# Kernel tuning notes

Measured on AMD Instinct MI355X. Metric: run time of the kernel, lower is better.

The kernel has to match this reference:

```python
import jax, jax.numpy as jnp
import numpy as np

B, N, M = 8, 2048, 2048
DQ = DK = DV = H = O = 1024

def setup_inputs() -> dict:
    key = jax.random.key(0)
    ks = jax.random.split(key, 10)
    input_query = jax.random.normal(ks[0], (B, N, DQ), dtype=jnp.float32)
    input_key = jax.random.normal(ks[1], (B, M, DK), dtype=jnp.float32)
    input_value = jax.random.normal(ks[2], (B, M, DV), dtype=jnp.float32)
    seq_lens = jax.random.randint(ks[3], (B,), 1, M + 1)
    seq_lens = seq_lens.at[0].set(M)  # original asserts max(seq_lens) == M
    s = 1.0 / np.sqrt(DQ)
    Wq = jax.random.normal(ks[4], (DQ, H), dtype=jnp.float32) * s
    bq = jnp.zeros((H,), dtype=jnp.float32)
    Wk = jax.random.normal(ks[5], (DK, H), dtype=jnp.float32) * s
    bk = jnp.zeros((H,), dtype=jnp.float32)
    Wv = jax.random.normal(ks[6], (DV, O), dtype=jnp.float32) * s
    bv = jnp.zeros((O,), dtype=jnp.float32)
    return {"input_query": input_query, "input_key": input_key, "input_value": input_value,
            "seq_lens": seq_lens, "Wq": Wq, "bq": bq, "Wk": Wk, "bk": bk, "Wv": Wv, "bv": bv}


def reference(input_query, input_key, input_value, seq_lens, Wq, bq, Wk, bk, Wv, bv):
    hidden_dim = Wq.shape[1]
    lq = input_query @ Wq + bq          # (B, N, H)
    lk = input_key @ Wk + bk            # (B, M, H)
    lv = input_value @ Wv + bv          # (B, M, O)
    scores = jnp.einsum('bnh,bmh->bnm', lq, lk) / jnp.sqrt(jnp.float32(hidden_dim))
    # additive mask: 0 for valid positions, finfo.min for padded (as in original)
    valid = (jnp.arange(scores.shape[-1]) < seq_lens[:, None])[:, None, :]  # (B,1,M)
    add_mask = jnp.where(valid, 0.0, jnp.finfo(scores.dtype).min)
    scores = scores + add_mask
    probs = jax.nn.softmax(scores, axis=-1)
    out = jnp.einsum('bnm,bmo->bno', probs, lv)  # dropout is identity in eval
    return out
```

## Files before the change

### kernel.cpp

```cpp
#include <hip/hip_runtime.h>
#include <hip/hip_bf16.h>

typedef unsigned short u16;
typedef __attribute__((ext_vector_type(8))) short bfrag;
typedef __attribute__((ext_vector_type(4))) float f32x4;
typedef __attribute__((ext_vector_type(8))) unsigned short us8;
typedef __attribute__((ext_vector_type(4))) unsigned short us4;

__device__ __forceinline__ u16 f2bf(float f) {
  union { float f; unsigned int u; } x; x.f = f;
  unsigned int r = x.u + 0x7fffu + ((x.u >> 16) & 1u);
  return (u16)(r >> 16);
}
__device__ __forceinline__ float bf2f(u16 u) {
  union { unsigned int u; float f; } x; x.u = ((unsigned int)u) << 16;
  return x.f;
}

__device__ __forceinline__ void gld16(const void* g, void* l) {
  __builtin_amdgcn_global_load_lds((const __attribute__((address_space(1))) void*)g,
                                   (__attribute__((address_space(3))) void*)l, 16, 0, 0);
}

__global__ __launch_bounds__(256) void transpose_w(const float* __restrict__ W0,
                                                   const float* __restrict__ W1,
                                                   const float* __restrict__ W2,
                                                   u16* __restrict__ T0,
                                                   u16* __restrict__ T1,
                                                   u16* __restrict__ T2) {
  const float* W = (blockIdx.z == 0) ? W0 : ((blockIdx.z == 1) ? W1 : W2);
  u16* T = (blockIdx.z == 0) ? T0 : ((blockIdx.z == 1) ? T1 : T2);
  __shared__ u16 tile[64][72];
  const int t = threadIdx.x;
  const int rr = t >> 4;
  const int cc = (t & 15) * 4;
  const int kbase = blockIdx.y * 64, nbase = blockIdx.x * 64;
#pragma unroll
  for (int j = 0; j < 4; ++j) {
    int kl = rr + j * 16;
    float4 v = *(const float4*)(W + (size_t)(kbase + kl) * 1024 + nbase + cc);
    tile[kl][cc + 0] = f2bf(v.x);
    tile[kl][cc + 1] = f2bf(v.y);
    tile[kl][cc + 2] = f2bf(v.z);
    tile[kl][cc + 3] = f2bf(v.w);
  }
  __syncthreads();
#pragma unroll
  for (int j = 0; j < 4; ++j) {
    int nl = rr + j * 16;
    us4 o;
    o[0] = tile[cc + 0][nl];
    o[1] = tile[cc + 1][nl];
    o[2] = tile[cc + 2][nl];
    o[3] = tile[cc + 3][nl];
    *(us4*)(T + (size_t)(nbase + nl) * 1024 + kbase + cc) = o;
  }
}

__global__ __launch_bounds__(256) void cvt_bf16(const float* __restrict__ src,
                                                u16* __restrict__ dst, int n8) {
  int i = blockIdx.x * blockDim.x + threadIdx.x;
  const int stride = gridDim.x * blockDim.x;
  for (; i < n8; i += stride) {
    const float4* p = (const float4*)(src + (size_t)i * 8);
    float4 v0 = p[0], v1 = p[1];
    us8 o;
    o[0] = f2bf(v0.x); o[1] = f2bf(v0.y); o[2] = f2bf(v0.z); o[3] = f2bf(v0.w);
    o[4] = f2bf(v1.x); o[5] = f2bf(v1.y); o[6] = f2bf(v1.z); o[7] = f2bf(v1.w);
    *(us8*)(dst + (size_t)i * 8) = o;
  }
}

template <int OUT>
__global__ __launch_bounds__(512, 2) void gemm256(const u16* __restrict__ gA,
                                                  const u16* __restrict__ gB,
                                                  const float* __restrict__ bias,
                                                  void* __restrict__ outp,
                                                  int K, int ldc,
                                                  size_t aStride, size_t bStride,
                                                  size_t cStride) {
  __shared__ u16 lds[65536];
  const int tid = threadIdx.x;
  const int z = blockIdx.z;
  const u16* A = gA + (size_t)z * aStride;
  const u16* B = gB + (size_t)z * bStride;
  const int brow = blockIdx.y * 256, bcol = blockIdx.x * 256;

  const int wv = tid >> 6, l = tid & 63;
  const int wm = wv >> 2, wn = wv & 3;
  const int fr = l & 15, fq = l >> 4;
  const int g0 = (fq ^ (fr & 7)) * 8;
  const int g1 = ((4 + fq) ^ (fr & 7)) * 8;

  const int srow = tid >> 3;
  const int sg = (tid & 7) ^ (srow & 7);
  const u16* aS = A + (size_t)(brow + srow) * K + sg * 8;
  const u16* bS = B + (size_t)(bcol + srow) * K + sg * 8;
  u16* const dA = lds + (tid >> 6) * 512;
  u16* const dB = lds + 32768 + (tid >> 6) * 512;

  f32x4 acc[8][4] = {};
  const int NT = K >> 6;

#pragma unroll
  for (int c = 0; c < 4; ++c) gld16(aS + (size_t)c * 64 * K, dA + c * 4096);
#pragma unroll
  for (int c = 0; c < 4; ++c) gld16(bS + (size_t)c * 64 * K, dB + c * 4096);
  asm volatile("s_waitcnt vmcnt(0)" ::: "memory");
  __builtin_amdgcn_s_barrier();

  for (int s = 0; s < NT; ++s) {
    const int cur = s & 1;
    const u16* At = lds + cur * 16384;
    const u16* Bt = lds + 32768 + cur * 16384;

    if (s + 1 < NT) {
      const int nb = cur ^ 1;
      const size_t ko = (size_t)(s + 1) * 64;
#pragma unroll
      for (int c = 0; c < 4; ++c)
        gld16(aS + ko + (size_t)c * 64 * K, dA + nb * 16384 + c * 4096);
#pragma unroll
      for (int c = 0; c < 4; ++c)
        gld16(bS + ko + (size_t)c * 64 * K, dB + nb * 16384 + c * 4096);
    }

    bfrag a[4][2], b[2][2][2];
#pragma unroll
    for (int m = 0; m < 4; ++m) {
      const u16* p = At + (wm * 128 + m * 16 + fr) * 64;
      a[m][0] = *(const bfrag*)(p + g0);
      a[m][1] = *(const bfrag*)(p + g1);
    }
#pragma unroll
    for (int n = 0; n < 2; ++n) {
      const u16* p = Bt + (wn * 64 + n * 16 + fr) * 64;
      b[0][n][0] = *(const bfrag*)(p + g0);
      b[0][n][1] = *(const bfrag*)(p + g1);
    }
    __builtin_amdgcn_s_barrier();
    __builtin_amdgcn_s_setprio(1);
#pragma unroll
    for (int n = 0; n < 2; ++n)
#pragma unroll
      for (int m = 0; m < 4; ++m) {
        acc[m][n] = __builtin_amdgcn_mfma_f32_16x16x32_bf16(a[m][0], b[0][n][0], acc[m][n], 0, 0, 0);
        acc[m][n] = __builtin_amdgcn_mfma_f32_16x16x32_bf16(a[m][1], b[0][n][1], acc[m][n], 0, 0, 0);
      }
    __builtin_amdgcn_s_setprio(0);
    __builtin_amdgcn_s_barrier();

#pragma unroll
    for (int n = 0; n < 2; ++n) {
      const u16* p = Bt + (wn * 64 + 32 + n * 16 + fr) * 64;
      b[1][n][0] = *(const bfrag*)(p + g0);
      b[1][n][1] = *(const bfrag*)(p + g1);
    }
    __builtin_amdgcn_s_barrier();
    __builtin_amdgcn_s_setprio(1);
#pragma unroll
    for (int n = 0; n < 2; ++n)
#pragma unroll
      for (int m = 0; m < 4; ++m) {
        acc[m][2 + n] = __builtin_amdgcn_mfma_f32_16x16x32_bf16(a[m][0], b[1][n][0], acc[m][2 + n], 0, 0, 0);
        acc[m][2 + n] = __builtin_amdgcn_mfma_f32_16x16x32_bf16(a[m][1], b[1][n][1], acc[m][2 + n], 0, 0, 0);
      }
    __builtin_amdgcn_s_setprio(0);
    __builtin_amdgcn_s_barrier();

#pragma unroll
    for (int m = 0; m < 4; ++m) {
      const u16* p = At + (wm * 128 + 64 + m * 16 + fr) * 64;
      a[m][0] = *(const bfrag*)(p + g0);
      a[m][1] = *(const bfrag*)(p + g1);
    }
    __builtin_amdgcn_s_barrier();
    __builtin_amdgcn_s_setprio(1);
#pragma unroll
    for (int n = 0; n < 2; ++n)
#pragma unroll
      for (int m = 0; m < 4; ++m) {
        acc[4 + m][n] = __builtin_amdgcn_mfma_f32_16x16x32_bf16(a[m][0], b[0][n][0], acc[4 + m][n], 0, 0, 0);
        acc[4 + m][n] = __builtin_amdgcn_mfma_f32_16x16x32_bf16(a[m][1], b[0][n][1], acc[4 + m][n], 0, 0, 0);
      }
    __builtin_amdgcn_s_setprio(0);
    __builtin_amdgcn_s_barrier();

    __builtin_amdgcn_s_setprio(1);
#pragma unroll
    for (int n = 0; n < 2; ++n)
#pragma unroll
      for (int m = 0; m < 4; ++m) {
        acc[4 + m][2 + n] = __builtin_amdgcn_mfma_f32_16x16x32_bf16(a[m][0], b[1][n][0], acc[4 + m][2 + n], 0, 0, 0);
        acc[4 + m][2 + n] = __builtin_amdgcn_mfma_f32_16x16x32_bf16(a[m][1], b[1][n][1], acc[4 + m][2 + n], 0, 0, 0);
      }
    __builtin_amdgcn_s_setprio(0);

    asm volatile("s_waitcnt vmcnt(0)" ::: "memory");
    __builtin_amdgcn_s_barrier();
  }

#pragma unroll
  for (int mg = 0; mg < 8; ++mg) {
    const int r0 = brow + wm * 128 + mg * 16 + fq * 4;
#pragma unroll
    for (int n = 0; n < 4; ++n) {
      const int c = bcol + wn * 64 + n * 16 + fr;
      f32x4 vv = acc[mg][n];
      if constexpr (OUT == 0) {
        float bb = bias[c];
        u16* C = (u16*)outp;
#pragma unroll
        for (int j = 0; j < 4; ++j) C[(size_t)(r0 + j) * ldc + c] = f2bf(vv[j] + bb);
      } else if constexpr (OUT == 1) {
        u16* C = (u16*)outp + (size_t)z * cStride;
#pragma unroll
        for (int j = 0; j < 4; ++j) C[(size_t)(r0 + j) * ldc + c] = f2bf(vv[j] * 0.03125f);
      } else if constexpr (OUT == 2) {
        float bb = bias[c];
        const int bz = r0 >> 11, mm = r0 & 2047;
        us4 o;
#pragma unroll
        for (int j = 0; j < 4; ++j) o[j] = f2bf(vv[j] + bb);
        *(us4*)((u16*)outp + ((size_t)bz * 1024 + c) * 2048 + mm) = o;
      } else {
        float* C = (float*)outp + (size_t)z * cStride;
#pragma unroll
        for (int j = 0; j < 4; ++j) C[(size_t)(r0 + j) * ldc + c] = vv[j];
      }
    }
  }
}

__global__ __launch_bounds__(256) void softmax_mask(u16* __restrict__ probs,
                                                    const int* __restrict__ seq) {
  const int bid = blockIdx.x;
  const int b = bid >> 11, n = bid & 2047;
  const int len = seq[b];
  u16* row = probs + ((size_t)b * 2048 + n) * 2048;
  const int t = threadIdx.x;
  const int w = t >> 6, l = t & 63;

  us8 sv = *(const us8*)(row + t * 8);
  float vals[8];
  float vmax = -1e30f;
#pragma unroll
  for (int e = 0; e < 8; ++e) {
    int m = t * 8 + e;
    float x = bf2f(sv[e]);
    vals[e] = (m < len) ? x : -1e30f;
    vmax = fmaxf(vmax, vals[e]);
  }
#pragma unroll
  for (int o = 32; o > 0; o >>= 1) vmax = fmaxf(vmax, __shfl_xor(vmax, o, 64));
  __shared__ float sm[4], ss[4];
  if (l == 0) sm[w] = vmax;
  __syncthreads();
  vmax = fmaxf(fmaxf(sm[0], sm[1]), fmaxf(sm[2], sm[3]));

  float ev[8];
  float sum = 0.f;
#pragma unroll
  for (int e = 0; e < 8; ++e) {
    int m = t * 8 + e;
    float p = (m < len) ? __expf(vals[e] - vmax) : 0.f;
    ev[e] = p;
    sum += p;
  }
#pragma unroll
  for (int o = 32; o > 0; o >>= 1) sum += __shfl_xor(sum, o, 64);
  if (l == 0) ss[w] = sum;
  __syncthreads();
  sum = ss[0] + ss[1] + ss[2] + ss[3];
  float inv = 1.f / sum;
  us8 ov;
#pragma unroll
  for (int e = 0; e < 8; ++e) ov[e] = f2bf(ev[e] * inv);
  *(us8*)(row + t * 8) = ov;
}

extern "C" void kernel_launch(void* const* d_in, const int* in_sizes, int n_in,
                              void* d_out, int out_size, void* d_ws, size_t ws_size,
                              hipStream_t stream) {
  const float* q   = (const float*)d_in[0];
  const float* k   = (const float*)d_in[1];
  const float* v   = (const float*)d_in[2];
  const int*   seq = (const int*)d_in[3];
  const float* Wq  = (const float*)d_in[4];
  const float* bq  = (const float*)d_in[5];
  const float* Wk  = (const float*)d_in[6];
  const float* bk  = (const float*)d_in[7];
  const float* Wv  = (const float*)d_in[8];
  const float* bv  = (const float*)d_in[9];
  float* out = (float*)d_out;

  u16* ws = (u16*)d_ws;
  u16* wtq = ws;
  u16* wtk = wtq + (size_t)1024 * 1024;
  u16* wtv = wtk + (size_t)1024 * 1024;
  u16* lq  = wtv + (size_t)1024 * 1024;
  u16* lk  = lq + (size_t)16384 * 1024;
  u16* lvt = lk + (size_t)16384 * 1024;
  u16* probs = lvt + (size_t)16384 * 1024;
  u16* cbuf = probs;

  const size_t S21 = (size_t)2048 * 1024;
  const size_t S22 = (size_t)2048 * 2048;

  transpose_w<<<dim3(16, 16, 3), 256, 0, stream>>>(Wq, Wk, Wv, wtq, wtk, wtv);

  cvt_bf16<<<dim3(2048), 256, 0, stream>>>(q, cbuf, 2097152);
  gemm256<0><<<dim3(4, 64, 1), 512, 0, stream>>>(cbuf, wtq, bq, lq, 1024, 1024, 0, 0, 0);
  cvt_bf16<<<dim3(2048), 256, 0, stream>>>(k, cbuf, 2097152);
  gemm256<0><<<dim3(4, 64, 1), 512, 0, stream>>>(cbuf, wtk, bk, lk, 1024, 1024, 0, 0, 0);
  cvt_bf16<<<dim3(2048), 256, 0, stream>>>(v, cbuf, 2097152);
  gemm256<2><<<dim3(4, 64, 1), 512, 0, stream>>>(cbuf, wtv, bv, lvt, 1024, 1024, 0, 0, 0);

  gemm256<1><<<dim3(8, 8, 8), 512, 0, stream>>>(lq, lk, nullptr, probs, 1024, 2048, S21, S21, S22);
  softmax_mask<<<dim3(16384), 256, 0, stream>>>(probs, seq);
  gemm256<3><<<dim3(4, 8, 8), 512, 0, stream>>>(probs, lvt, nullptr, out, 2048, 1024, S22, S21, S21);
}
```

Before: 347.0 us.

## Remap GEMM workgroups per XCD and interleave next-tile loads across compute phases

Workgroup IDs are remapped so consecutive logical tiles land on the same XCD, which should improve L2 reuse of shared A/B panels. The global-to-LDS prefetch is no longer issued in one batch per iteration. It is split into chunks spread between the MFMA phases, loads run up to two tiles ahead, and a partial vmcnt wait replaces the full drain at the end of each iteration. This is meant to hide memory latency and cut the pipeline bubble, at the cost of tricky buffer reuse: the t+2 loads write into the current buffer while other waves may still be reading it.

New measurement: 335.1 us. 1.04x faster.

```diff
diff --git a/kernel.cpp b/kernel.cpp
--- a/kernel.cpp
+++ b/kernel.cpp
@@ -81,10 +81,22 @@
                                                   size_t cStride) {
   __shared__ u16 lds[65536];
   const int tid = threadIdx.x;
-  const int z = blockIdx.z;
-  const u16* A = gA + (size_t)z * aStride;
-  const u16* B = gB + (size_t)z * bStride;
-  const int brow = blockIdx.y * 256, bcol = blockIdx.x * 256;
+
+  const int gx = gridDim.x, gy = gridDim.y;
+  const int nwg = gx * gy * gridDim.z;
+  int orig = blockIdx.x + gx * (blockIdx.y + gy * blockIdx.z);
+  {
+    const int qq = nwg >> 3, rr2 = nwg & 7;
+    const int xcd = orig & 7, idx = orig >> 3;
+    orig = (xcd < rr2 ? xcd * (qq + 1) : rr2 * (qq + 1) + (xcd - rr2) * qq) + idx;
+  }
+  const int bx = orig % gx;
+  const int tmp_ = orig / gx;
+  const int by = tmp_ % gy, bz = tmp_ / gy;
+
+  const u16* A = gA + (size_t)bz * aStride;
+  const u16* B = gB + (size_t)bz * bStride;
+  const int brow = by * 256, bcol = bx * 256;
 
   const int wv = tid >> 6, l = tid & 63;
   const int wm = wv >> 2, wn = wv & 3;
@@ -96,36 +108,39 @@
   const int sg = (tid & 7) ^ (srow & 7);
   const u16* aS = A + (size_t)(brow + srow) * K + sg * 8;
   const u16* bS = B + (size_t)(bcol + srow) * K + sg * 8;
-  u16* const dA = lds + (tid >> 6) * 512;
-  u16* const dB = lds + 32768 + (tid >> 6) * 512;
+  u16* const dA = lds + wv * 512;
+  u16* const dB = lds + 32768 + wv * 512;
 
   f32x4 acc[8][4] = {};
   const int NT = K >> 6;
 
-#pragma unroll
-  for (int c = 0; c < 4; ++c) gld16(aS + (size_t)c * 64 * K, dA + c * 4096);
-#pragma unroll
-  for (int c = 0; c < 4; ++c) gld16(bS + (size_t)c * 64 * K, dB + c * 4096);
-  asm volatile("s_waitcnt vmcnt(0)" ::: "memory");
-  __builtin_amdgcn_s_barrier();
-
-  for (int s = 0; s < NT; ++s) {
-    const int cur = s & 1;
+  auto stA = [&](int tile, int c, int buf) {
+    gld16(aS + (size_t)tile * 64 + (size_t)c * 64 * K, dA + buf * 16384 + c * 4096);
+  };
+  auto stB = [&](int tile, int c, int buf) {
+    gld16(bS + (size_t)tile * 64 + (size_t)c * 64 * K, dB + buf * 16384 + c * 4096);
+  };
+
+#pragma unroll
+  for (int c = 0; c < 4; ++c) stA(0, c, 0);
+#pragma unroll
+  for (int c = 0; c < 4; ++c) stB(0, c, 0);
+  if (NT > 1) {
+    stA(1, 0, 1); stA(1, 2, 1);
+    stB(1, 0, 1); stB(1, 1, 1); stB(1, 2, 1); stB(1, 3, 1);
+  }
+
+  for (int t = 0; t < NT; ++t) {
+    const int cur = t & 1;
     const u16* At = lds + cur * 16384;
     const u16* Bt = lds + 32768 + cur * 16384;
 
-    if (s + 1 < NT) {
-      const int nb = cur ^ 1;
-      const size_t ko = (size_t)(s + 1) * 64;
-#pragma unroll
-      for (int c = 0; c < 4; ++c)
-        gld16(aS + ko + (size_t)c * 64 * K, dA + nb * 16384 + c * 4096);
-#pragma unroll
-      for (int c = 0; c < 4; ++c)
-        gld16(bS + ko + (size_t)c * 64 * K, dB + nb * 16384 + c * 4096);
-    }
+    if (t + 1 < NT) asm volatile("s_waitcnt vmcnt(6)" ::: "memory");
+    else            asm volatile("s_waitcnt vmcnt(0)" ::: "memory");
+    __builtin_amdgcn_s_barrier();
 
     bfrag a[4][2], b[2][2][2];
+
 #pragma unroll
     for (int m = 0; m < 4; ++m) {
       const u16* p = At + (wm * 128 + m * 16 + fr) * 64;
@@ -138,6 +153,7 @@
       b[0][n][0] = *(const bfrag*)(p + g0);
       b[0][n][1] = *(const bfrag*)(p + g1);
     }
+    if (t + 1 < NT) { stA(t + 1, 1, cur ^ 1); stA(t + 1, 3, cur ^ 1); }
     __builtin_amdgcn_s_barrier();
     __builtin_amdgcn_s_setprio(1);
 #pragma unroll
@@ -156,6 +172,7 @@
       b[1][n][0] = *(const bfrag*)(p + g0);
       b[1][n][1] = *(const bfrag*)(p + g1);
     }
+    if (t + 2 < NT) { stA(t + 2, 0, cur); stA(t + 2, 2, cur); }
     __builtin_amdgcn_s_barrier();
     __builtin_amdgcn_s_setprio(1);
 #pragma unroll
@@ -174,6 +191,7 @@
       a[m][0] = *(const bfrag*)(p + g0);
       a[m][1] = *(const bfrag*)(p + g1);
     }
+    if (t + 2 < NT) { stB(t + 2, 0, cur); stB(t + 2, 1, cur); }
     __builtin_amdgcn_s_barrier();
     __builtin_amdgcn_s_setprio(1);
 #pragma unroll
@@ -186,6 +204,7 @@
     __builtin_amdgcn_s_setprio(0);
     __builtin_amdgcn_s_barrier();
 
+    if (t + 2 < NT) { stB(t + 2, 2, cur); stB(t + 2, 3, cur); }
     __builtin_amdgcn_s_setprio(1);
 #pragma unroll
     for (int n = 0; n < 2; ++n)
@@ -195,8 +214,6 @@
         acc[4 + m][2 + n] = __builtin_amdgcn_mfma_f32_16x16x32_bf16(a[m][1], b[1][n][1], acc[4 + m][2 + n], 0, 0, 0);
       }
     __builtin_amdgcn_s_setprio(0);
-
-    asm volatile("s_waitcnt vmcnt(0)" ::: "memory");
     __builtin_amdgcn_s_barrier();
   }
 
@@ -213,18 +230,18 @@
 #pragma unroll
         for (int j = 0; j < 4; ++j) C[(size_t)(r0 + j) * ldc + c] = f2bf(vv[j] + bb);
       } else if constexpr (OUT == 1) {
-        u16* C = (u16*)outp + (size_t)z * cStride;
+        u16* C = (u16*)outp + (size_t)bz * cStride;
 #pragma unroll
         for (int j = 0; j < 4; ++j) C[(size_t)(r0 + j) * ldc + c] = f2bf(vv[j] * 0.03125f);
       } else if constexpr (OUT == 2) {
         float bb = bias[c];
-        const int bz = r0 >> 11, mm = r0 & 2047;
+        const int bz2 = r0 >> 11, mm = r0 & 2047;
         us4 o;
 #pragma unroll
         for (int j = 0; j < 4; ++j) o[j] = f2bf(vv[j] + bb);
-        *(us4*)((u16*)outp + ((size_t)bz * 1024 + c) * 2048 + mm) = o;
+        *(us4*)((u16*)outp + ((size_t)bz2 * 1024 + c) * 2048 + mm) = o;
       } else {
-        float* C = (float*)outp + (size_t)z * cStride;
+        float* C = (float*)outp + (size_t)bz * cStride;
 #pragma unroll
         for (int j = 0; j < 4; ++j) C[(size_t)(r0 + j) * ldc + c] = vv[j];
       }
```
